# Kernel optimization log

Measured on AMD Instinct MI355X. Metric: run time of the kernel, lower is better.

## Reference

```python
import jax, jax.numpy as jnp
import numpy as np

EPS = 1e-6  # flax nnx LayerNorm default

def _ln(x):
    # LayerNorm without scale/bias
    m = jnp.mean(x, axis=-1, keepdims=True)
    v = jnp.mean(jnp.square(x - m), axis=-1, keepdims=True)
    return (x - m) * jax.lax.rsqrt(v + EPS)

def _modulate(x, shift, scale):
    return x * (1.0 + scale[:, None]) + shift[:, None]

def setup_inputs() -> dict:
    key = jax.random.key(0)
    B, S, H, NH = 8, 1024, 1024, 16
    ks = jax.random.split(key, 12)
    s = lambda k, sh: jax.random.normal(k, sh, dtype=jnp.float32) * 0.02
    return {
        "x": jax.random.normal(ks[0], (B, S, H), dtype=jnp.float32),
        "c": jax.random.normal(ks[1], (B, H), dtype=jnp.float32),
        "w_ada": s(ks[2], (H, 6 * H)),
        "b_ada": jnp.zeros((6 * H,), dtype=jnp.float32),
        "w_qkv": s(ks[3], (H, 3 * H)),
        "w_proj": s(ks[4], (H, H)),
        "b_proj": jnp.zeros((H,), dtype=jnp.float32),
        "w_mlp1": s(ks[5], (H, 4 * H)),
        "b_mlp1": jnp.zeros((4 * H,), dtype=jnp.float32),
        "w_mlp2": s(ks[6], (4 * H, H)),
        "b_mlp2": jnp.zeros((H,), dtype=jnp.float32),
    }

def reference(x, c, w_ada, b_ada, w_qkv, w_proj, b_proj, w_mlp1, b_mlp1, w_mlp2, b_mlp2):
    B, S, H = x.shape
    NH = 16
    CH = H // NH
    # adaLN modulation: silu -> Linear
    cmod = jax.nn.silu(c) @ w_ada + b_ada  # [B, 6H]
    shift_msa, scale_msa, gate_msa, shift_mlp, scale_mlp, gate_mlp = jnp.split(cmod, 6, axis=-1)
    # attention branch
    x_mod = _modulate(_ln(x), shift_msa, scale_msa)
    qkv = x_mod @ w_qkv  # [B, S, 3H]
    k, q, v = jnp.split(qkv, 3, axis=-1)  # note source order: k, q, v
    k = k.reshape(B, S, NH, CH)
    q = q.reshape(B, S, NH, CH)
    v = v.reshape(B, S, NH, CH)
    q = q / CH  # faithful: divide by head_dim (not sqrt)
    w = jnp.einsum('bqhc,bkhc->bhqk', q, k).astype(jnp.float32)
    w = jax.nn.softmax(w, axis=-1)
    y = jnp.einsum('bhqk,bkhc->bqhc', w, v).reshape(B, S, H)
    attn_x = y @ w_proj + b_proj
    x = x + gate_msa[:, None] * attn_x
    # MLP branch
    x_mod2 = _modulate(_ln(x), shift_mlp, scale_mlp)
    h = jax.nn.gelu(x_mod2 @ w_mlp1 + b_mlp1)
    mlp_x = h @ w_mlp2 + b_mlp2
    x = x + gate_mlp[:, None] * mlp_x
    return x
```

## Files before the change

### kernel.cpp

```cpp
#include <hip/hip_runtime.h>
#include <stdint.h>

typedef unsigned short u16;
using bf16x8 = __attribute__((ext_vector_type(8))) __bf16;
using f32x4  = __attribute__((ext_vector_type(4))) float;

#define MFMA16(a,b,c) __builtin_amdgcn_mfma_f32_16x16x32_bf16((a),(b),(c),0,0,0)

__device__ __forceinline__ u16 f2bf(float f) {
  union { float f; uint32_t u; } v; v.f = f;
  uint32_t r = v.u + 0x7FFFu + ((v.u >> 16) & 1u);
  return (u16)(r >> 16);
}

__device__ __forceinline__ void gload_lds16(const void* g, void* l) {
  typedef const __attribute__((address_space(1))) void* gp_t;
  typedef __attribute__((address_space(3))) void* lp_t;
  __builtin_amdgcn_global_load_lds((gp_t)(uintptr_t)g,
                                   (lp_t)(uint32_t)(uintptr_t)l, 16, 0, 0);
}

__global__ __launch_bounds__(256)
void adaln_part_k(const float* __restrict__ c, const float* __restrict__ w,
                  float* __restrict__ partial) {
  const int jb = blockIdx.x, ks = blockIdx.y;
  const int j = jb * 256 + threadIdx.x;
  __shared__ float sil[8][32];
  {
    int b = threadIdx.x >> 5, kk = threadIdx.x & 31;
    float v = c[b * 1024 + ks * 32 + kk];
    sil[b][kk] = v / (1.f + __expf(-v));
  }
  __syncthreads();
  float acc[8] = {0,0,0,0,0,0,0,0};
#pragma unroll 8
  for (int kk = 0; kk < 32; ++kk) {
    float wv = w[(size_t)(ks * 32 + kk) * 6144 + j];
#pragma unroll
    for (int b = 0; b < 8; ++b) acc[b] += sil[b][kk] * wv;
  }
#pragma unroll
  for (int b = 0; b < 8; ++b)
    partial[((size_t)ks * 8 + b) * 6144 + j] = acc[b];
}

__global__ __launch_bounds__(256)
void adaln_red_k(const float* __restrict__ partial, const float* __restrict__ bias,
                 float* __restrict__ cmod) {
  int g = blockIdx.x * 256 + threadIdx.x;
  int j = g % 6144;
  float s = bias[j];
#pragma unroll 8
  for (int ks = 0; ks < 32; ++ks)
    s += partial[(size_t)ks * 8 * 6144 + g];
  cmod[g] = s;
}

__global__ __launch_bounds__(256)
void tcast_k(const float* __restrict__ in, u16* __restrict__ out, int K, int N,
             int lo, int hi, float scale) {
  __shared__ u16 t[64][65];
  int n0 = blockIdx.x * 64, k0 = blockIdx.y * 64;
#pragma unroll
  for (int i = 0; i < 16; ++i) {
    int idx = i * 256 + threadIdx.x;
    int r = idx >> 6, cc = idx & 63;
    float v = in[(size_t)(k0 + r) * N + n0 + cc];
    int n = n0 + cc;
    if (n >= lo && n < hi) v *= scale;
    t[r][cc] = f2bf(v);
  }
  __syncthreads();
#pragma unroll
  for (int i = 0; i < 16; ++i) {
    int idx = i * 256 + threadIdx.x;
    int r = idx >> 6, cc = idx & 63;
    out[(size_t)(n0 + r) * K + k0 + cc] = t[cc][r];
  }
}

__global__ __launch_bounds__(256)
void lnmod_k(const float* __restrict__ x, const float* __restrict__ cmod,
             int shift_off, int scale_off, u16* __restrict__ out) {
  int row = blockIdx.x;
  int b = row >> 10;
  const float4* xr = (const float4*)(x + (size_t)row * 1024);
  float4 v = xr[threadIdx.x];
  float s = v.x + v.y + v.z + v.w;
  float sq = v.x * v.x + v.y * v.y + v.z * v.z + v.w * v.w;
#pragma unroll
  for (int m = 32; m >= 1; m >>= 1) {
    s  += __shfl_xor(s, m);
    sq += __shfl_xor(sq, m);
  }
  __shared__ float ss[4], ssq[4];
  int wave = threadIdx.x >> 6, lane = threadIdx.x & 63;
  if (lane == 0) { ss[wave] = s; ssq[wave] = sq; }
  __syncthreads();
  s  = ss[0] + ss[1] + ss[2] + ss[3];
  sq = ssq[0] + ssq[1] + ssq[2] + ssq[3];
  float mean = s * (1.f / 1024.f);
  float var  = sq * (1.f / 1024.f) - mean * mean;
  float rstd = rsqrtf(var + 1e-6f);
  int col = threadIdx.x * 4;
  const float* sh = cmod + (size_t)b * 6144 + shift_off + col;
  const float* sc = cmod + (size_t)b * 6144 + scale_off + col;
  float xv[4] = {v.x, v.y, v.z, v.w};
  union { u16 o[4]; uint64_t u; } pk;
#pragma unroll
  for (int j = 0; j < 4; ++j)
    pk.o[j] = f2bf((xv[j] - mean) * rstd * (1.f + sc[j]) + sh[j]);
  *(uint64_t*)(out + (size_t)row * 1024 + col) = pk.u;
}

__global__ __launch_bounds__(256)
void tv_k(const u16* __restrict__ qkv, u16* __restrict__ vt) {
  __shared__ u16 t[64][65];
  int r0 = blockIdx.x * 64;
  int h = blockIdx.y;
  int b = r0 >> 10;
  int s0 = r0 & 1023;
#pragma unroll
  for (int i = 0; i < 16; ++i) {
    int idx = i * 256 + threadIdx.x;
    int r = idx >> 6, cc = idx & 63;
    t[r][cc] = qkv[(size_t)(r0 + r) * 3072 + 2048 + h * 64 + cc];
  }
  __syncthreads();
#pragma unroll
  for (int i = 0; i < 16; ++i) {
    int idx = i * 256 + threadIdx.x;
    int ch = idx >> 6, scc = idx & 63;
    vt[((size_t)(b * 16 + h) * 64 + ch) * 1024 + s0 + scc] = t[scc][ch];
  }
}

__device__ __forceinline__ float gelu_f(float x) {
  float z = 1.5957691216057308f * (x + 0.044715f * x * x * x);
  return x / (1.f + __expf(-z));
}

template <int EP>
__global__ __launch_bounds__(512, 2)
void gemm8_k(const u16* __restrict__ A, const u16* __restrict__ Bt,
             int N, int K,
             const float* __restrict__ bias, const float* __restrict__ resid,
             const float* __restrict__ gate, void* __restrict__ outp) {
  __shared__ __align__(16) u16 As[2][256 * 64];
  __shared__ __align__(16) u16 Bs[2][256 * 64];
  const int bn = blockIdx.x, bm = blockIdx.y;
  const int tid = threadIdx.x;
  const int wave = tid >> 6, lane = tid & 63;
  const int l15 = lane & 15, lhi = lane >> 4;
  const int wm = wave >> 2, wn = wave & 3;
  const int nkt = K >> 6;
  const size_t arow0 = (size_t)bm * 256;
  const size_t brow0 = (size_t)bn * 256;

  f32x4 acc[8][4] = {};

  auto stage_half = [&](const u16* mat, size_t row0, u16* dst, int kt) {
    const u16* src = mat + row0 * K + (size_t)kt * 64;
#pragma unroll
    for (int i = 0; i < 2; ++i) {
      int q = i * 512 + tid;
      int r = q >> 3, cc = (q & 7) ^ (r & 7);
      gload_lds16(src + (size_t)r * K + cc * 8, dst + (i * 8 + wave) * 512);
    }
  };
  auto lda = [&](int cur, int row, int kh) -> bf16x8 {
    int cc = (kh * 4 + lhi) ^ (row & 7);
    return *(const bf16x8*)&As[cur][row * 64 + cc * 8];
  };
  auto ldb = [&](int cur, int row, int kh) -> bf16x8 {
    int cc = (kh * 4 + lhi) ^ (row & 7);
    return *(const bf16x8*)&Bs[cur][row * 64 + cc * 8];
  };

  stage_half(A, arow0,       &As[0][0],        0);
  stage_half(A, arow0 + 128, &As[0][128 * 64], 0);
  stage_half(Bt, brow0,       &Bs[0][0],        0);
  stage_half(Bt, brow0 + 128, &Bs[0][128 * 64], 0);
  stage_half(A, arow0,       &As[1][0],        1);
  stage_half(A, arow0 + 128, &As[1][128 * 64], 1);
  stage_half(Bt, brow0,       &Bs[1][0],        1);
  stage_half(Bt, brow0 + 128, &Bs[1][128 * 64], 1);
  asm volatile("s_waitcnt vmcnt(8)" ::: "memory");
  __builtin_amdgcn_s_barrier();

  bf16x8 afr[4][2], bfr[4][2];
  for (int kt = 0; kt < nkt; ++kt) {
    const int cur = kt & 1;
    const bool pf = (kt + 2 < nkt);

#pragma unroll
    for (int m = 0; m < 4; ++m) {
      int r = wm * 128 + m * 16 + l15;
      afr[m][0] = lda(cur, r, 0); afr[m][1] = lda(cur, r, 1);
    }
#pragma unroll
    for (int n = 0; n < 2; ++n) {
      int r = wn * 64 + n * 16 + l15;
      bfr[n][0] = ldb(cur, r, 0); bfr[n][1] = ldb(cur, r, 1);
    }
    __builtin_amdgcn_s_barrier();
    __builtin_amdgcn_s_setprio(1);
#pragma unroll
    for (int m = 0; m < 4; ++m)
#pragma unroll
      for (int n = 0; n < 2; ++n) {
        acc[m][n] = MFMA16(afr[m][0], bfr[n][0], acc[m][n]);
        acc[m][n] = MFMA16(afr[m][1], bfr[n][1], acc[m][n]);
      }
    __builtin_amdgcn_s_setprio(0);
    __builtin_amdgcn_s_barrier();

#pragma unroll
    for (int n = 2; n < 4; ++n) {
      int r = wn * 64 + n * 16 + l15;
      bfr[n][0] = ldb(cur, r, 0); bfr[n][1] = ldb(cur, r, 1);
    }
    __builtin_amdgcn_s_barrier();
    __builtin_amdgcn_s_setprio(1);
#pragma unroll
    for (int m = 0; m < 4; ++m)
#pragma unroll
      for (int n = 2; n < 4; ++n) {
        acc[m][n] = MFMA16(afr[m][0], bfr[n][0], acc[m][n]);
        acc[m][n] = MFMA16(afr[m][1], bfr[n][1], acc[m][n]);
      }
    __builtin_amdgcn_s_setprio(0);
    __builtin_amdgcn_s_barrier();

#pragma unroll
    for (int m = 0; m < 4; ++m) {
      int r = wm * 128 + 64 + m * 16 + l15;
      afr[m][0] = lda(cur, r, 0); afr[m][1] = lda(cur, r, 1);
    }
    if (pf) {
      stage_half(Bt, brow0,       &Bs[cur][0],        kt + 2);
      stage_half(Bt, brow0 + 128, &Bs[cur][128 * 64], kt + 2);
    }
    __builtin_amdgcn_s_barrier();
    __builtin_amdgcn_s_setprio(1);
#pragma unroll
    for (int m = 0; m < 4; ++m)
#pragma unroll
      for (int n = 0; n < 2; ++n) {
        acc[m + 4][n] = MFMA16(afr[m][0], bfr[n][0], acc[m + 4][n]);
        acc[m + 4][n] = MFMA16(afr[m][1], bfr[n][1], acc[m + 4][n]);
      }
    __builtin_amdgcn_s_setprio(0);
    __builtin_amdgcn_s_barrier();

    if (pf) {
      stage_half(A, arow0,       &As[cur][0],        kt + 2);
      stage_half(A, arow0 + 128, &As[cur][128 * 64], kt + 2);
    }
    __builtin_amdgcn_s_barrier();
    __builtin_amdgcn_s_setprio(1);
#pragma unroll
    for (int m = 0; m < 4; ++m)
#pragma unroll
      for (int n = 2; n < 4; ++n) {
        acc[m + 4][n] = MFMA16(afr[m][0], bfr[n][0], acc[m + 4][n]);
        acc[m + 4][n] = MFMA16(afr[m][1], bfr[n][1], acc[m + 4][n]);
      }
    __builtin_amdgcn_s_setprio(0);
    if (kt + 1 < nkt) {
      if (pf) asm volatile("s_waitcnt vmcnt(8)" ::: "memory");
      else    asm volatile("s_waitcnt vmcnt(0)" ::: "memory");
      __builtin_amdgcn_s_barrier();
    }
  }

#pragma unroll
  for (int m = 0; m < 8; ++m) {
    int row = bm * 256 + wm * 128 + m * 16 + lhi * 4;
#pragma unroll
    for (int n = 0; n < 4; ++n) {
      int col = bn * 256 + wn * 64 + n * 16 + l15;
#pragma unroll
      for (int r = 0; r < 4; ++r) {
        int rr = row + r;
        float v = acc[m][n][r];
        if (EP == 0) {
          ((u16*)outp)[(size_t)rr * N + col] = f2bf(v);
        } else if (EP == 1) {
          ((u16*)outp)[(size_t)rr * N + col] = f2bf(gelu_f(v + bias[col]));
        } else {
          float t2 = v + bias[col];
          int b = rr >> 10;
          float res = resid[(size_t)rr * N + col];
          ((float*)outp)[(size_t)rr * N + col] = res + gate[(size_t)b * 6144 + col] * t2;
        }
      }
    }
  }
}

__global__ __launch_bounds__(256)
void attn_k(const u16* __restrict__ qkv, const u16* __restrict__ vt,
            u16* __restrict__ y) {
  const int qt = blockIdx.x, h = blockIdx.y, b = blockIdx.z;
  const int tid = threadIdx.x, wave = tid >> 6, lane = tid & 63;
  const int l15 = lane & 15, lhi = lane >> 4;
  __shared__ __align__(16) u16 Qs[64 * 64];
  __shared__ __align__(16) u16 Ks[2][64 * 64];
  __shared__ __align__(16) u16 Vs[2][64 * 64];
  __shared__ __align__(16) u16 Ps[64 * 64];
  const size_t qrow0 = (size_t)b * 1024 + qt * 64;
  const size_t krow0 = (size_t)b * 1024;
  const size_t vrow0 = (size_t)(b * 16 + h) * 64;

  auto stageQ = [&]() {
#pragma unroll
    for (int i = 0; i < 2; ++i) {
      int c = (i * 4 + wave) * 64 + lane;
      int r = c >> 3, j = (c & 7) ^ (c >> 3 & 7);
      gload_lds16(qkv + (qrow0 + r) * 3072 + 1024 + h * 64 + j * 8,
                  &Qs[(i * 4 + wave) * 512]);
    }
  };
  auto stageKV = [&](int buf, int kt) {
#pragma unroll
    for (int i = 0; i < 2; ++i) {
      int c = (i * 4 + wave) * 64 + lane;
      int r = c >> 3, j = (c & 7) ^ (c >> 3 & 7);
      gload_lds16(qkv + (krow0 + kt * 64 + r) * 3072 + h * 64 + j * 8,
                  &Ks[buf][(i * 4 + wave) * 512]);
      gload_lds16(vt + (vrow0 + r) * 1024 + kt * 64 + j * 8,
                  &Vs[buf][(i * 4 + wave) * 512]);
    }
  };
  auto ldb = [](const u16* base, int row, int cc) -> bf16x8 {
    return *(const bf16x8*)&base[row * 64 + ((cc ^ (row & 7)) << 3)];
  };

  stageQ();
  stageKV(0, 0);
  __syncthreads();
  bf16x8 qf[2];
  qf[0] = ldb(Qs, wave * 16 + l15, lhi);
  qf[1] = ldb(Qs, wave * 16 + l15, 4 + lhi);

  bf16x8 ones;
#pragma unroll
  for (int j = 0; j < 8; ++j) ones[j] = (__bf16)1.0f;

  float m_r[4];
  f32x4 o[5] = {};
#pragma unroll
  for (int r = 0; r < 4; ++r) m_r[r] = -3.0e38f;

  for (int kt = 0; kt < 16; ++kt) {
    int cur = kt & 1;
    if (kt < 15) stageKV(cur ^ 1, kt + 1);
    f32x4 sf[4] = {};
    __builtin_amdgcn_s_setprio(1);
#pragma unroll
    for (int n = 0; n < 4; ++n) {
      bf16x8 k0 = ldb(Ks[cur], n * 16 + l15, lhi);
      bf16x8 k1 = ldb(Ks[cur], n * 16 + l15, 4 + lhi);
      sf[n] = MFMA16(qf[0], k0, sf[n]);
      sf[n] = MFMA16(qf[1], k1, sf[n]);
    }
    __builtin_amdgcn_s_setprio(0);
#pragma unroll
    for (int r = 0; r < 4; ++r) {
      float mx = fmaxf(fmaxf(sf[0][r], sf[1][r]), fmaxf(sf[2][r], sf[3][r]));
      mx = fmaxf(mx, __shfl_xor(mx, 1));
      mx = fmaxf(mx, __shfl_xor(mx, 2));
      mx = fmaxf(mx, __shfl_xor(mx, 4));
      mx = fmaxf(mx, __shfl_xor(mx, 8));
      float mn = fmaxf(m_r[r], mx);
      float al = __expf(m_r[r] - mn);
      m_r[r] = mn;
      float p0 = __expf(sf[0][r] - mn);
      float p1 = __expf(sf[1][r] - mn);
      float p2 = __expf(sf[2][r] - mn);
      float p3 = __expf(sf[3][r] - mn);
      o[0][r] *= al; o[1][r] *= al; o[2][r] *= al; o[3][r] *= al; o[4][r] *= al;
      int row = wave * 16 + lhi * 4 + r;
      int rb = row * 64, sw = (row & 7) << 3;
      Ps[rb + (l15 ^ sw)]        = f2bf(p0);
      Ps[rb + ((l15 + 16) ^ sw)] = f2bf(p1);
      Ps[rb + ((l15 + 32) ^ sw)] = f2bf(p2);
      Ps[rb + ((l15 + 48) ^ sw)] = f2bf(p3);
    }
    bf16x8 pf0 = ldb(Ps, wave * 16 + l15, lhi);
    bf16x8 pf1 = ldb(Ps, wave * 16 + l15, 4 + lhi);
    __builtin_amdgcn_s_setprio(1);
#pragma unroll
    for (int n = 0; n < 4; ++n) {
      bf16x8 v0 = ldb(Vs[cur], n * 16 + l15, lhi);
      bf16x8 v1 = ldb(Vs[cur], n * 16 + l15, 4 + lhi);
      o[n] = MFMA16(pf0, v0, o[n]);
      o[n] = MFMA16(pf1, v1, o[n]);
    }
    o[4] = MFMA16(pf0, ones, o[4]);
    o[4] = MFMA16(pf1, ones, o[4]);
    __builtin_amdgcn_s_setprio(0);
    __syncthreads();
  }
#pragma unroll
  for (int r = 0; r < 4; ++r) {
    float inv = 1.0f / o[4][r];
    size_t yrow = (qrow0 + wave * 16 + lhi * 4 + r) * 1024 + h * 64 + l15;
    y[yrow]      = f2bf(o[0][r] * inv);
    y[yrow + 16] = f2bf(o[1][r] * inv);
    y[yrow + 32] = f2bf(o[2][r] * inv);
    y[yrow + 48] = f2bf(o[3][r] * inv);
  }
}

extern "C" void kernel_launch(void* const* d_in, const int* in_sizes, int n_in,
                              void* d_out, int out_size, void* d_ws, size_t ws_size,
                              hipStream_t stream) {
  const float* x      = (const float*)d_in[0];
  const float* c      = (const float*)d_in[1];
  const float* w_ada  = (const float*)d_in[2];
  const float* b_ada  = (const float*)d_in[3];
  const float* w_qkv  = (const float*)d_in[4];
  const float* w_proj = (const float*)d_in[5];
  const float* b_proj = (const float*)d_in[6];
  const float* w_mlp1 = (const float*)d_in[7];
  const float* b_mlp1 = (const float*)d_in[8];
  const float* w_mlp2 = (const float*)d_in[9];
  const float* b_mlp2 = (const float*)d_in[10];
  float* out = (float*)d_out;

  char* ws = (char*)d_ws;
  size_t off = 0;
  auto alloc = [&](size_t bytes) {
    void* p = ws + off;
    off += (bytes + 255) & ~(size_t)255;
    return p;
  };
  float* cmod  = (float*)alloc((size_t)8 * 6144 * 4);
  float* apart = (float*)alloc((size_t)32 * 8 * 6144 * 4);
  u16* wqkvT   = (u16*)alloc((size_t)3072 * 1024 * 2);
  u16* wprojT  = (u16*)alloc((size_t)1024 * 1024 * 2);
  u16* wmlp1T  = (u16*)alloc((size_t)4096 * 1024 * 2);
  u16* wmlp2T  = (u16*)alloc((size_t)1024 * 4096 * 2);
  u16* xmod    = (u16*)alloc((size_t)8192 * 1024 * 2);
  u16* qkv     = (u16*)alloc((size_t)8192 * 3072 * 2);
  u16* vt      = (u16*)alloc((size_t)8 * 16 * 64 * 1024 * 2);
  float* x1    = (float*)alloc((size_t)8192 * 1024 * 4);
  u16* hbuf    = (u16*)alloc((size_t)8192 * 4096 * 2);
  u16* ybuf  = xmod;
  u16* xmod2 = qkv;

  adaln_part_k<<<dim3(24, 32), 256, 0, stream>>>(c, w_ada, apart);
  adaln_red_k<<<192, 256, 0, stream>>>(apart, b_ada, cmod);
  tcast_k<<<dim3(3072 / 64, 1024 / 64), 256, 0, stream>>>(w_qkv,  wqkvT,  1024, 3072,
                                                          1024, 2048, 1.0f / 64.0f);
  tcast_k<<<dim3(1024 / 64, 1024 / 64), 256, 0, stream>>>(w_proj, wprojT, 1024, 1024, 0, 0, 1.f);
  tcast_k<<<dim3(4096 / 64, 1024 / 64), 256, 0, stream>>>(w_mlp1, wmlp1T, 1024, 4096, 0, 0, 1.f);
  tcast_k<<<dim3(1024 / 64, 4096 / 64), 256, 0, stream>>>(w_mlp2, wmlp2T, 4096, 1024, 0, 0, 1.f);
  lnmod_k<<<8192, 256, 0, stream>>>(x, cmod, 0, 1024, xmod);
  gemm8_k<0><<<dim3(3072 / 256, 8192 / 256), 512, 0, stream>>>(
      xmod, wqkvT, 3072, 1024, nullptr, nullptr, nullptr, qkv);
  tv_k<<<dim3(128, 16), 256, 0, stream>>>(qkv, vt);
  attn_k<<<dim3(16, 16, 8), 256, 0, stream>>>(qkv, vt, ybuf);
  gemm8_k<2><<<dim3(1024 / 256, 8192 / 256), 512, 0, stream>>>(
      ybuf, wprojT, 1024, 1024, b_proj, x, cmod + 2048, x1);
  lnmod_k<<<8192, 256, 0, stream>>>(x1, cmod, 3072, 4096, xmod2);
  gemm8_k<1><<<dim3(4096 / 256, 8192 / 256), 512, 0, stream>>>(
      xmod2, wmlp1T, 4096, 1024, b_mlp1, nullptr, nullptr, hbuf);
  gemm8_k<2><<<dim3(1024 / 256, 8192 / 256), 512, 0, stream>>>(
      hbuf, wmlp2T, 1024, 4096, b_mlp2, x1, cmod + 5120, out);
}
```

Before: 459.1 us.

## Software-pipeline LDS fragment loads across k-steps and swizzle GEMM block order

```diff
diff --git a/kernel.cpp b/kernel.cpp
--- a/kernel.cpp
+++ b/kernel.cpp
@@ -148,7 +148,10 @@
              const float* __restrict__ gate, void* __restrict__ outp) {
   __shared__ __align__(16) u16 As[2][256 * 64];
   __shared__ __align__(16) u16 Bs[2][256 * 64];
-  const int bn = blockIdx.x, bm = blockIdx.y;
+  const int nwg = gridDim.x * gridDim.y;
+  int bid = blockIdx.y * gridDim.x + blockIdx.x;
+  int swz = (bid & 7) * (nwg >> 3) + (bid >> 3);
+  const int bn = swz % gridDim.x, bm = swz / gridDim.x;
   const int tid = threadIdx.x;
   const int wave = tid >> 6, lane = tid & 63;
   const int l15 = lane & 15, lhi = lane >> 4;
@@ -177,101 +180,112 @@
     return *(const bf16x8*)&Bs[cur][row * 64 + cc * 8];
   };
 
-  stage_half(A, arow0,       &As[0][0],        0);
-  stage_half(A, arow0 + 128, &As[0][128 * 64], 0);
+  stage_half(A,  arow0,       &As[0][0],        0);
+  stage_half(A,  arow0 + 128, &As[0][128 * 64], 0);
   stage_half(Bt, brow0,       &Bs[0][0],        0);
   stage_half(Bt, brow0 + 128, &Bs[0][128 * 64], 0);
-  stage_half(A, arow0,       &As[1][0],        1);
-  stage_half(A, arow0 + 128, &As[1][128 * 64], 1);
+  stage_half(A,  arow0,       &As[1][0],        1);
+  stage_half(A,  arow0 + 128, &As[1][128 * 64], 1);
   stage_half(Bt, brow0,       &Bs[1][0],        1);
   stage_half(Bt, brow0 + 128, &Bs[1][128 * 64], 1);
   asm volatile("s_waitcnt vmcnt(8)" ::: "memory");
   __builtin_amdgcn_s_barrier();
 
-  bf16x8 afr[4][2], bfr[4][2];
+  bf16x8 A1[4][2], A2[4][2], B1[2][2], B2[2][2];
+#pragma unroll
+  for (int m = 0; m < 4; ++m) {
+    int r = wm * 128 + m * 16 + l15;
+    A1[m][0] = lda(0, r, 0); A1[m][1] = lda(0, r, 1);
+  }
+#pragma unroll
+  for (int n = 0; n < 2; ++n) {
+    int r = wn * 64 + n * 16 + l15;
+    B1[n][0] = ldb(0, r, 0); B1[n][1] = ldb(0, r, 1);
+  }
+
   for (int kt = 0; kt < nkt; ++kt) {
-    const int cur = kt & 1;
-    const bool pf = (kt + 2 < nkt);
-
-#pragma unroll
-    for (int m = 0; m < 4; ++m) {
-      int r = wm * 128 + m * 16 + l15;
-      afr[m][0] = lda(cur, r, 0); afr[m][1] = lda(cur, r, 1);
-    }
+    const int cur = kt & 1, oth = cur ^ 1;
+    const bool nxt = (kt + 1 < nkt), pf2 = (kt + 2 < nkt);
+
+    __builtin_amdgcn_s_barrier();
 #pragma unroll
     for (int n = 0; n < 2; ++n) {
-      int r = wn * 64 + n * 16 + l15;
-      bfr[n][0] = ldb(cur, r, 0); bfr[n][1] = ldb(cur, r, 1);
-    }
+      int r = wn * 64 + 32 + n * 16 + l15;
+      B2[n][0] = ldb(cur, r, 0); B2[n][1] = ldb(cur, r, 1);
+    }
+    __builtin_amdgcn_s_setprio(1);
+#pragma unroll
+    for (int m = 0; m < 4; ++m)
+#pragma unroll
+      for (int n = 0; n < 2; ++n) {
+        acc[m][n] = MFMA16(A1[m][0], B1[n][0], acc[m][n]);
+        acc[m][n] = MFMA16(A1[m][1], B1[n][1], acc[m][n]);
+      }
+    __builtin_amdgcn_s_setprio(0);
+
     __builtin_amdgcn_s_barrier();
-    __builtin_amdgcn_s_setprio(1);
-#pragma unroll
-    for (int m = 0; m < 4; ++m)
-#pragma unroll
-      for (int n = 0; n < 2; ++n) {
-        acc[m][n] = MFMA16(afr[m][0], bfr[n][0], acc[m][n]);
-        acc[m][n] = MFMA16(afr[m][1], bfr[n][1], acc[m][n]);
-      }
-    __builtin_amdgcn_s_setprio(0);
-    __builtin_amdgcn_s_barrier();
-
-#pragma unroll
-    for (int n = 2; n < 4; ++n) {
-      int r = wn * 64 + n * 16 + l15;
-      bfr[n][0] = ldb(cur, r, 0); bfr[n][1] = ldb(cur, r, 1);
-    }
-    __builtin_amdgcn_s_barrier();
-    __builtin_amdgcn_s_setprio(1);
-#pragma unroll
-    for (int m = 0; m < 4; ++m)
-#pragma unroll
-      for (int n = 2; n < 4; ++n) {
-        acc[m][n] = MFMA16(afr[m][0], bfr[n][0], acc[m][n]);
-        acc[m][n] = MFMA16(afr[m][1], bfr[n][1], acc[m][n]);
-      }
-    __builtin_amdgcn_s_setprio(0);
-    __builtin_amdgcn_s_barrier();
-
+    if (pf2) {
+      stage_half(Bt, brow0,       &Bs[cur][0],        kt + 2);
+      stage_half(Bt, brow0 + 128, &Bs[cur][128 * 64], kt + 2);
+    }
 #pragma unroll
     for (int m = 0; m < 4; ++m) {
       int r = wm * 128 + 64 + m * 16 + l15;
-      afr[m][0] = lda(cur, r, 0); afr[m][1] = lda(cur, r, 1);
-    }
-    if (pf) {
-      stage_half(Bt, brow0,       &Bs[cur][0],        kt + 2);
-      stage_half(Bt, brow0 + 128, &Bs[cur][128 * 64], kt + 2);
-    }
+      A2[m][0] = lda(cur, r, 0); A2[m][1] = lda(cur, r, 1);
+    }
+    __builtin_amdgcn_s_setprio(1);
+#pragma unroll
+    for (int m = 0; m < 4; ++m)
+#pragma unroll
+      for (int n = 0; n < 2; ++n) {
+        acc[m][n + 2] = MFMA16(A1[m][0], B2[n][0], acc[m][n + 2]);
+        acc[m][n + 2] = MFMA16(A1[m][1], B2[n][1], acc[m][n + 2]);
+      }
+    __builtin_amdgcn_s_setprio(0);
+
     __builtin_amdgcn_s_barrier();
-    __builtin_amdgcn_s_setprio(1);
-#pragma unroll
-    for (int m = 0; m < 4; ++m)
-#pragma unroll
-      for (int n = 0; n < 2; ++n) {
-        acc[m + 4][n] = MFMA16(afr[m][0], bfr[n][0], acc[m + 4][n]);
-        acc[m + 4][n] = MFMA16(afr[m][1], bfr[n][1], acc[m + 4][n]);
-      }
-    __builtin_amdgcn_s_setprio(0);
-    __builtin_amdgcn_s_barrier();
-
-    if (pf) {
+    if (nxt) {
+      if (pf2) asm volatile("s_waitcnt vmcnt(4)" ::: "memory");
+      else     asm volatile("s_waitcnt vmcnt(0)" ::: "memory");
+    }
+    if (pf2) {
       stage_half(A, arow0,       &As[cur][0],        kt + 2);
       stage_half(A, arow0 + 128, &As[cur][128 * 64], kt + 2);
     }
+    if (nxt) {
+#pragma unroll
+      for (int m = 0; m < 4; ++m) {
+        int r = wm * 128 + m * 16 + l15;
+        A1[m][0] = lda(oth, r, 0); A1[m][1] = lda(oth, r, 1);
+      }
+    }
+    __builtin_amdgcn_s_setprio(1);
+#pragma unroll
+    for (int m = 0; m < 4; ++m)
+#pragma unroll
+      for (int n = 0; n < 2; ++n) {
+        acc[m + 4][n] = MFMA16(A2[m][0], B1[n][0], acc[m + 4][n]);
+        acc[m + 4][n] = MFMA16(A2[m][1], B1[n][1], acc[m + 4][n]);
+      }
+    __builtin_amdgcn_s_setprio(0);
+
     __builtin_amdgcn_s_barrier();
+    if (nxt) {
+#pragma unroll
+      for (int n = 0; n < 2; ++n) {
+        int r = wn * 64 + n * 16 + l15;
+        B1[n][0] = ldb(oth, r, 0); B1[n][1] = ldb(oth, r, 1);
+      }
+    }
     __builtin_amdgcn_s_setprio(1);
 #pragma unroll
     for (int m = 0; m < 4; ++m)
 #pragma unroll
-      for (int n = 2; n < 4; ++n) {
-        acc[m + 4][n] = MFMA16(afr[m][0], bfr[n][0], acc[m + 4][n]);
-        acc[m + 4][n] = MFMA16(afr[m][1], bfr[n][1], acc[m + 4][n]);
-      }
-    __builtin_amdgcn_s_setprio(0);
-    if (kt + 1 < nkt) {
-      if (pf) asm volatile("s_waitcnt vmcnt(8)" ::: "memory");
-      else    asm volatile("s_waitcnt vmcnt(0)" ::: "memory");
-      __builtin_amdgcn_s_barrier();
-    }
+      for (int n = 0; n < 2; ++n) {
+        acc[m + 4][n + 2] = MFMA16(A2[m][0], B2[n][0], acc[m + 4][n + 2]);
+        acc[m + 4][n + 2] = MFMA16(A2[m][1], B2[n][1], acc[m + 4][n + 2]);
+      }
+    __builtin_amdgcn_s_setprio(0);
   }
 
 #pragma unroll
```

Measured after the change: 437.1 us. 1.05x faster.
